# Performance work log

Measured on AMD Instinct MI355X. Metric: run time of the kernel, lower is better.

## Reference

```python
import jax, jax.numpy as jnp
import numpy as np

NUM_LAYERS = 6
D = 16           # physical_dim == bond_dim (required for multi-layer consistency)
B, S, FIN = 128, 2048, 128


def setup_inputs() -> dict:
    key = jax.random.key(0)
    k0, k1, k2, k3 = jax.random.split(key, 4)
    return {
        "sequence": jax.random.normal(k0, (B, S, FIN), jnp.float32),
        "W_emb": jax.random.normal(k1, (FIN, D), jnp.float32) * 0.05,
        "b_emb": jnp.zeros((D,), jnp.float32),
        "u": jax.random.normal(k2, (NUM_LAYERS, D, D, D, D), jnp.float32) * 0.1,
        "w": jax.random.normal(k3, (NUM_LAYERS, D, D, D), jnp.float32) * 0.1,
    }


def _ent_entropy(sA, sB):
    # sA: (B, pA, d), sB: (B, pB, d)
    corr = jnp.einsum('bik,bjk->bij', sA, sB)          # (B, pA, pB)
    s = jnp.linalg.svd(corr, compute_uv=False)          # (B, min(pA,pB))
    sn = s / (jnp.sum(s, axis=1, keepdims=True) + 1e-8)
    return -jnp.sum(sn * jnp.log(sn + 1e-8), axis=1)    # (B,)


def _phi_q(sites):
    # sites: (B, n, d), n >= 4 and even
    n = sites.shape[1]
    mid = n // 2
    S_int = _ent_entropy(sites[:, :mid], sites[:, mid:])
    A, Bp = sites[:, :mid], sites[:, mid:]
    S1 = _ent_entropy(A[:, :mid // 2], A[:, mid // 2:])
    S2 = _ent_entropy(Bp[:, :(n - mid) // 2], Bp[:, (n - mid) // 2:])
    return jnp.maximum(S_int - (S1 + S2), 0.0)


def _apply_layer(sites, u_l, w_l):
    # sites: (B, n, d) with n even. Disentangle adjacent pairs, then coarse-grain.
    b, n, d = sites.shape
    s = sites.reshape(b, n // 2, 2, d)
    # disentangler: einsum('ijkl,bi,bj->bkl') batched over pairs p
    comb = jnp.einsum('ijkl,bpi,bpj->bpkl', u_l, s[:, :, 0], s[:, :, 1])
    o1 = comb.mean(axis=3)   # mean over l -> (b, p, k)
    o2 = comb.mean(axis=2)   # mean over k -> (b, p, l)
    # isometry acts on consecutive disentangled pairs (o1_i, o2_i)
    return jnp.einsum('aij,bpi,bpj->bpa', w_l, o1, o2)  # (b, n//2, bond)


def reference(sequence, W_emb, b_emb, u, w):
    emb = sequence @ W_emb + b_emb                       # (B, S, D)
    norm = jnp.linalg.norm(emb, axis=-1, keepdims=True)
    sites = emb / jnp.maximum(norm, 1e-12)               # F.normalize(dim=-1)
    for l in range(NUM_LAYERS):
        sites = _apply_layer(sites, u[l], w[l])
    phi_q = _phi_q(sites)
    return sites, phi_q
```

## Files before the change

### kernel.cpp

```cpp
#include <hip/hip_runtime.h>
#include <hip/hip_bf16.h>
#include <math.h>

#define BATCH 128
#define SEQ   2048
#define FIN   128
#define DD    16
#define NLAYERS 6
#define SST   20

#define BUFA_F  (BATCH*SEQ*DD)
#define BUFB_F  (BATCH*(SEQ/2)*DD)
#define COEF_OFF (BUFA_F + BUFB_F)
#define ENT_OFF  (COEF_OFF + NLAYERS*12288)

__global__ __launch_bounds__(256) void k_prep(const float* __restrict__ u,
                                              const float* __restrict__ w,
                                              float* __restrict__ coef) {
    int l  = blockIdx.x;
    int ij = threadIdx.x;
    const float* ub = u + (size_t)l*65536 + (size_t)ij*256;
    float a1[16], a2[16];
#pragma unroll
    for (int k = 0; k < 16; ++k) { a1[k] = 0.0f; a2[k] = 0.0f; }
#pragma unroll
    for (int k = 0; k < 16; ++k) {
#pragma unroll
        for (int z = 0; z < 16; ++z) {
            float v = ub[k*16 + z];
            a1[k] += v;
            a2[z] += v;
        }
    }
    float* ucb = coef + (size_t)l*12288 + ij*32;
#pragma unroll
    for (int k = 0; k < 16; ++k) {
        ucb[k]      = a1[k]*(1.0f/16.0f);
        ucb[16 + k] = a2[k]*(1.0f/16.0f);
    }
    const float* wb = w + (size_t)l*4096;
    float* wtb = coef + (size_t)l*12288 + 8192 + ij*16;
#pragma unroll
    for (int a = 0; a < 16; ++a) wtb[a] = wb[a*256 + ij];
}

__global__ __launch_bounds__(256) void k_embed(const float* __restrict__ seq,
                                               const float* __restrict__ W,
                                               const float* __restrict__ bias,
                                               float* __restrict__ out) {
    __shared__ float wl[2048];
    int t = threadIdx.x;
    for (int x = t; x < 2048; x += 256) wl[x] = W[x];
    int q = t & 3;
    size_t row = ((size_t)blockIdx.x*256 + t) >> 2;
    float acc[4];
    {
        float4 bv = *(const float4*)(bias + q*4);
        acc[0] = bv.x; acc[1] = bv.y; acc[2] = bv.z; acc[3] = bv.w;
    }
    __syncthreads();

    const float4* rp = (const float4*)seq + row*32;
#pragma unroll 8
    for (int kk = 0; kk < 32; ++kk) {
        float4 rv = rp[kk];
        float rc[4] = { rv.x, rv.y, rv.z, rv.w };
#pragma unroll
        for (int c = 0; c < 4; ++c) {
            float4 wv = *(const float4*)&wl[(kk*4 + c)*16 + q*4];
            float s = rc[c];
            acc[0] = fmaf(s, wv.x, acc[0]);
            acc[1] = fmaf(s, wv.y, acc[1]);
            acc[2] = fmaf(s, wv.z, acc[2]);
            acc[3] = fmaf(s, wv.w, acc[3]);
        }
    }
    float p = 0.0f;
#pragma unroll
    for (int j = 0; j < 4; ++j) p = fmaf(acc[j], acc[j], p);
    p += __shfl_xor(p, 1);
    p += __shfl_xor(p, 2);
    float inv = 1.0f / fmaxf(sqrtf(p), 1e-12f);
    *(float4*)(out + row*16 + q*4) = make_float4(acc[0]*inv, acc[1]*inv,
                                                 acc[2]*inv, acc[3]*inv);
}

__global__ __launch_bounds__(256) void k_layer(const float* __restrict__ in,
                                               float* __restrict__ outp,
                                               const float* __restrict__ coefl) {
    __shared__ float cbuf[8192];
    __shared__ float spl[64*36];
    int t = threadIdx.x;
    int og = t & 7, pg = t >> 3;
    int lane = t & 63, base = lane & ~7;

    const float4* wtf = (const float4*)(coefl + 8192);
    float4 wr0 = wtf[0*256 + t];
    float4 wr1 = wtf[1*256 + t];
    float4 wr2 = wtf[2*256 + t];
    float4 wr3 = wtf[3*256 + t];

    {
        const float4* ucf = (const float4*)coefl;
        float4* c4 = (float4*)cbuf;
#pragma unroll
        for (int it = 0; it < 8; ++it) c4[it*256 + t] = ucf[it*256 + t];
    }
    {
        const float4* ing = (const float4*)in + (size_t)blockIdx.x*512;
        float4 v0 = ing[t];
        float4 v1 = ing[t + 256];
        *(float4*)&spl[(t >> 3)*36 + (t & 7)*4]        = v0;
        *(float4*)&spl[((t >> 3) + 32)*36 + (t & 7)*4] = v1;
    }
    __syncthreads();

    float s1v[2][16];
#pragma unroll
    for (int pp = 0; pp < 2; ++pp) {
        int p = pg + pp*32;
#pragma unroll
        for (int g = 0; g < 4; ++g) {
            float4 v = *(const float4*)&spl[p*36 + 16 + g*4];
            s1v[pp][g*4+0]=v.x; s1v[pp][g*4+1]=v.y; s1v[pp][g*4+2]=v.z; s1v[pp][g*4+3]=v.w;
        }
    }

    float accv[2][4];
    accv[0][0]=0.f; accv[0][1]=0.f; accv[0][2]=0.f; accv[0][3]=0.f;
    accv[1][0]=0.f; accv[1][1]=0.f; accv[1][2]=0.f; accv[1][3]=0.f;

    for (int i = 0; i < 16; ++i) {
        float s0a = spl[pg*36 + i];
        float s0b = spl[(pg + 32)*36 + i];
        const float4* uc = (const float4*)&cbuf[i*512] + og;
#pragma unroll
        for (int j = 0; j < 16; ++j) {
            float4 cv = uc[j*8];
            float pa = s0a * s1v[0][j];
            float pb = s0b * s1v[1][j];
            accv[0][0] = fmaf(pa, cv.x, accv[0][0]);
            accv[0][1] = fmaf(pa, cv.y, accv[0][1]);
            accv[0][2] = fmaf(pa, cv.z, accv[0][2]);
            accv[0][3] = fmaf(pa, cv.w, accv[0][3]);
            accv[1][0] = fmaf(pb, cv.x, accv[1][0]);
            accv[1][1] = fmaf(pb, cv.y, accv[1][1]);
            accv[1][2] = fmaf(pb, cv.z, accv[1][2]);
            accv[1][3] = fmaf(pb, cv.w, accv[1][3]);
        }
    }
    __syncthreads();
    {
        float4* c4 = (float4*)cbuf;
        c4[0*256 + t] = wr0;
        c4[1*256 + t] = wr1;
        c4[2*256 + t] = wr2;
        c4[3*256 + t] = wr3;
    }
    __syncthreads();

    float o2f[2][16];
#pragma unroll
    for (int j = 0; j < 16; ++j) {
        int src = base + 4 + (j >> 2);
        o2f[0][j] = __shfl(accv[0][j & 3], src, 64);
        o2f[1][j] = __shfl(accv[1][j & 3], src, 64);
    }

    float r0a = 0.f, r1a = 0.f, r0b = 0.f, r1b = 0.f;
    for (int grp = 0; grp < 4; ++grp) {
#pragma unroll
        for (int c = 0; c < 4; ++c) {
            float o1a = __shfl(accv[0][c], base + grp, 64);
            float o1b = __shfl(accv[1][c], base + grp, 64);
            const float2* wrow = (const float2*)&cbuf[(grp*4 + c)*256] + og;
#pragma unroll
            for (int j = 0; j < 16; ++j) {
                float2 wv = wrow[j*8];
                float qa = o1a * o2f[0][j];
                float qb = o1b * o2f[1][j];
                r0a = fmaf(qa, wv.x, r0a);
                r1a = fmaf(qa, wv.y, r1a);
                r0b = fmaf(qb, wv.x, r0b);
                r1b = fmaf(qb, wv.y, r1b);
            }
        }
    }

    size_t gp = (size_t)blockIdx.x*64;
    *(float2*)&outp[(gp + pg)*16 + og*2]      = make_float2(r0a, r1a);
    *(float2*)&outp[(gp + pg + 32)*16 + og*2] = make_float2(r0b, r1b);
}

template<int P, bool LAST>
__device__ __forceinline__ void layer_body(float* sL, const float* coef,
                                           float* outp, int npg, int t, int bid) {
    int og = t & 7, pg = t >> 3;
    int lane = t & 63, base = lane & ~7;
    bool act = pg < npg;

    float accv[P][4];
    float s1v[P][16];
#pragma unroll
    for (int pp = 0; pp < P; ++pp) { accv[pp][0]=0.f; accv[pp][1]=0.f; accv[pp][2]=0.f; accv[pp][3]=0.f; }

    if (act) {
#pragma unroll
        for (int pp = 0; pp < P; ++pp) {
            int r = 2*(pg + pp*32) + 1;
#pragma unroll
            for (int g = 0; g < 4; ++g) {
                float4 v = *(const float4*)&sL[r*SST + g*4];
                s1v[pp][g*4+0]=v.x; s1v[pp][g*4+1]=v.y; s1v[pp][g*4+2]=v.z; s1v[pp][g*4+3]=v.w;
            }
        }
        for (int i = 0; i < 16; ++i) {
            float s0[P];
#pragma unroll
            for (int pp = 0; pp < P; ++pp) s0[pp] = sL[(2*(pg + pp*32))*SST + i];
            const float4* uc = (const float4*)&coef[i*512] + og;
#pragma unroll
            for (int j = 0; j < 16; ++j) {
                float4 cv = uc[j*8];
#pragma unroll
                for (int pp = 0; pp < P; ++pp) {
                    float p = s0[pp] * s1v[pp][j];
                    accv[pp][0] = fmaf(p, cv.x, accv[pp][0]);
                    accv[pp][1] = fmaf(p, cv.y, accv[pp][1]);
                    accv[pp][2] = fmaf(p, cv.z, accv[pp][2]);
                    accv[pp][3] = fmaf(p, cv.w, accv[pp][3]);
                }
            }
        }
    }
    __syncthreads();

    if (act) {
        float o2f[P][16];
#pragma unroll
        for (int j = 0; j < 16; ++j) {
            int src = base + 4 + (j >> 2);
#pragma unroll
            for (int pp = 0; pp < P; ++pp)
                o2f[pp][j] = __shfl(accv[pp][j & 3], src, 64);
        }
        float r0[P], r1[P];
#pragma unroll
        for (int pp = 0; pp < P; ++pp) { r0[pp] = 0.f; r1[pp] = 0.f; }
        for (int grp = 0; grp < 4; ++grp) {
#pragma unroll
            for (int c = 0; c < 4; ++c) {
                float o1i[P];
#pragma unroll
                for (int pp = 0; pp < P; ++pp)
                    o1i[pp] = __shfl(accv[pp][c], base + grp, 64);
#pragma unroll
                for (int j = 0; j < 16; ++j) {
                    float2 wv = *(const float2*)&coef[8192 + ((grp*4+c)*16 + j)*16 + og*2];
#pragma unroll
                    for (int pp = 0; pp < P; ++pp) {
                        float q = o1i[pp] * o2f[pp][j];
                        r0[pp] = fmaf(q, wv.x, r0[pp]);
                        r1[pp] = fmaf(q, wv.y, r1[pp]);
                    }
                }
            }
        }
        if (LAST) {
#pragma unroll
            for (int pp = 0; pp < P; ++pp) {
                int p = pg + pp*32;
                *(float2*)&outp[((size_t)bid*32 + p)*16 + og*2] = make_float2(r0[pp], r1[pp]);
            }
        } else {
#pragma unroll
            for (int pp = 0; pp < P; ++pp) {
                int p = pg + pp*32;
                *(float2*)&sL[p*SST + og*2] = make_float2(r0[pp], r1[pp]);
            }
        }
    }
    __syncthreads();
}

__global__ __launch_bounds__(256) void k_tail(const float* __restrict__ in,
                                              const float* __restrict__ coefg,
                                              float* __restrict__ outp) {
    __shared__ float coef[12288];
    __shared__ float sL[256*SST];
    int t = threadIdx.x, bid = blockIdx.x;

    const float4* in4 = (const float4*)in + (size_t)bid*1024;
#pragma unroll
    for (int it = 0; it < 4; ++it) {
        int f = it*256 + t;
        *(float4*)&sL[(f >> 2)*SST + (f & 3)*4] = in4[f];
    }
#pragma unroll 1
    for (int l = 0; l < 3; ++l) {
        const float4* src = (const float4*)(coefg + (size_t)(3 + l)*12288);
        __syncthreads();
        for (int x = t; x < 3072; x += 256) ((float4*)coef)[x] = src[x];
        __syncthreads();
        switch (l) {
            case 0: layer_body<4,false>(sL, coef, outp, 32, t, bid); break;
            case 1: layer_body<2,false>(sL, coef, outp, 32, t, bid); break;
            case 2: layer_body<1,true >(sL, coef, outp, 32, t, bid); break;
        }
    }
}

__device__ __forceinline__ void rot_cs(float al, float be, float ga, float& c, float& s) {
    float ze = (be - al) / (2.0f * ga);
    float tt = copysignf(1.0f, ze) / (fabsf(ze) + sqrtf(1.0f + ze*ze));
    c = 1.0f / sqrtf(1.0f + tt*tt);
    s = c * tt;
}

__global__ __launch_bounds__(64) void k_phi(const float* __restrict__ sites,
                                            float* __restrict__ ent) {
    __shared__ float S[512];
    __shared__ float C[256];
    __shared__ float sv[16];
    int bid = blockIdx.x;
    int role = bid >> 7;
    int b = bid & 127;
    int t = threadIdx.x;
    const float* sp = sites + (size_t)b*512;

    if (role == 0) {
        for (int x = t; x < 512; x += 64) S[x] = sp[x];
        __syncthreads();
        for (int e = t; e < 256; e += 64) {
            int i = e & 15, j = e >> 4;
            float a = 0.0f;
            for (int k = 0; k < 16; ++k) a = fmaf(S[i*16+k], S[(16+j)*16+k], a);
            C[j*16 + i] = a;
        }
        __syncthreads();
        for (int sw = 0; sw < 12; ++sw) {
            for (int r = 0; r < 15; ++r) {
                int pr = t >> 3, sub = t & 7;
                int p, q;
                if (pr == 0) { p = 15; q = r; }
                else { p = (r + pr) % 15; q = (r + 15 - pr) % 15; }
                float u0 = C[p*16 + 2*sub],   u1v = C[p*16 + 2*sub + 1];
                float v0 = C[q*16 + 2*sub],   v1v = C[q*16 + 2*sub + 1];
                float al = u0*u0 + u1v*u1v;
                float be = v0*v0 + v1v*v1v;
                float ga = u0*v0 + u1v*v1v;
                al += __shfl_xor(al,1); al += __shfl_xor(al,2); al += __shfl_xor(al,4);
                be += __shfl_xor(be,1); be += __shfl_xor(be,2); be += __shfl_xor(be,4);
                ga += __shfl_xor(ga,1); ga += __shfl_xor(ga,2); ga += __shfl_xor(ga,4);
                if (ga != 0.0f) {
                    float c, s; rot_cs(al, be, ga, c, s);
                    C[p*16 + 2*sub]     = fmaf(c, u0, -s*v0);
                    C[p*16 + 2*sub + 1] = fmaf(c, u1v, -s*v1v);
                    C[q*16 + 2*sub]     = fmaf(s, u0,  c*v0);
                    C[q*16 + 2*sub + 1] = fmaf(s, u1v, c*v1v);
                }
                __syncthreads();
            }
        }
        if (t < 16) {
            float s2 = 0.0f;
            for (int rr = 0; rr < 16; ++rr) { float v = C[t*16+rr]; s2 = fmaf(v, v, s2); }
            sv[t] = sqrtf(s2);
        }
        __syncthreads();
        if (t == 0) {
            float sum = 0.0f;
            for (int i2 = 0; i2 < 16; ++i2) sum += sv[i2];
            float den = sum + 1e-8f;
            float e2 = 0.0f;
            for (int i2 = 0; i2 < 16; ++i2) {
                float sn = sv[i2] / den;
                e2 -= sn * logf(sn + 1e-8f);
            }
            ent[b] = e2;
        }
    } else {
        int ro = (role == 1) ? 0 : 256;
        for (int x = t; x < 256; x += 64) S[x] = sp[ro + x];
        __syncthreads();
        if (t < 64) {
            int i = t & 7, j = t >> 3;
            float a = 0.0f;
            for (int k = 0; k < 16; ++k) a = fmaf(S[i*16+k], S[(8+j)*16+k], a);
            C[j*8 + i] = a;
        }
        __syncthreads();
        for (int sw = 0; sw < 12; ++sw) {
            for (int r = 0; r < 7; ++r) {
                if (t < 32) {
                    int pr = t >> 3, sub = t & 7;
                    int p, q;
                    if (pr == 0) { p = 7; q = r; }
                    else { p = (r + pr) % 7; q = (r + 7 - pr) % 7; }
                    float uu = C[p*8 + sub], vv = C[q*8 + sub];
                    float al = uu*uu, be = vv*vv, ga = uu*vv;
                    al += __shfl_xor(al,1); al += __shfl_xor(al,2); al += __shfl_xor(al,4);
                    be += __shfl_xor(be,1); be += __shfl_xor(be,2); be += __shfl_xor(be,4);
                    ga += __shfl_xor(ga,1); ga += __shfl_xor(ga,2); ga += __shfl_xor(ga,4);
                    if (ga != 0.0f) {
                        float c, s; rot_cs(al, be, ga, c, s);
                        C[p*8 + sub] = fmaf(c, uu, -s*vv);
                        C[q*8 + sub] = fmaf(s, uu,  c*vv);
                    }
                }
                __syncthreads();
            }
        }
        if (t < 8) {
            float s2 = 0.0f;
            for (int rr = 0; rr < 8; ++rr) { float v = C[t*8+rr]; s2 = fmaf(v, v, s2); }
            sv[t] = sqrtf(s2);
        }
        __syncthreads();
        if (t == 0) {
            float sum = 0.0f;
            for (int i2 = 0; i2 < 8; ++i2) sum += sv[i2];
            float den = sum + 1e-8f;
            float e2 = 0.0f;
            for (int i2 = 0; i2 < 8; ++i2) {
                float sn = sv[i2] / den;
                e2 -= sn * logf(sn + 1e-8f);
            }
            ent[role*128 + b] = e2;
        }
    }
}

__global__ __launch_bounds__(128) void k_phi2(const float* __restrict__ ent,
                                              float* __restrict__ phi) {
    int b = threadIdx.x;
    phi[b] = fmaxf(ent[b] - (ent[128 + b] + ent[256 + b]), 0.0f);
}

extern "C" void kernel_launch(void* const* d_in, const int* in_sizes, int n_in,
                              void* d_out, int out_size, void* d_ws, size_t ws_size,
                              hipStream_t stream) {
    const float* seq  = (const float*)d_in[0];
    const float* W    = (const float*)d_in[1];
    const float* bias = (const float*)d_in[2];
    const float* u    = (const float*)d_in[3];
    const float* w    = (const float*)d_in[4];
    float* out = (float*)d_out;
    float* ws  = (float*)d_ws;

    float* bufA  = ws;
    float* bufB  = ws + BUFA_F;
    float* coefw = ws + COEF_OFF;
    float* entb  = ws + ENT_OFF;

    k_prep <<<NLAYERS, 256, 0, stream>>>(u, w, coefw);
    k_embed<<<(BATCH*SEQ*4)/256, 256, 0, stream>>>(seq, W, bias, bufA);

    k_layer<<<2048, 256, 0, stream>>>(bufA, bufB, coefw + 0*12288);
    k_layer<<<1024, 256, 0, stream>>>(bufB, bufA, coefw + 1*12288);
    k_layer<<< 512, 256, 0, stream>>>(bufA, bufB, coefw + 2*12288);
    k_tail <<< 128, 256, 0, stream>>>(bufB, coefw, out);

    k_phi <<<3*BATCH, 64, 0, stream>>>(out, entb);
    k_phi2<<<1, 128, 0, stream>>>(entb, out + BATCH*32*DD);
}
```

Baseline: 232.3 us.

## Merge prep into embed kernel, stage rows in LDS, cut Jacobi sweeps

Folds the coefficient-prep kernel into the embedding kernel as six extra blocks, removing one launch. The embedding now loads 64 input rows per block into padded shared memory with coalesced float4 reads, instead of each thread striding through global memory. The one-sided Jacobi SVD sweep count in the phi kernel also drops from 12 to 8, which risks less converged singular values. The larger shared-memory footprint per block may lower occupancy in the bandwidth-bound embed stage.

```diff
diff --git a/kernel.cpp b/kernel.cpp
--- a/kernel.cpp
+++ b/kernel.cpp
@@ -8,51 +8,63 @@
 #define DD    16
 #define NLAYERS 6
 #define SST   20
+#define SWEEPS 8
 
 #define BUFA_F  (BATCH*SEQ*DD)
 #define BUFB_F  (BATCH*(SEQ/2)*DD)
 #define COEF_OFF (BUFA_F + BUFB_F)
 #define ENT_OFF  (COEF_OFF + NLAYERS*12288)
 
-__global__ __launch_bounds__(256) void k_prep(const float* __restrict__ u,
-                                              const float* __restrict__ w,
-                                              float* __restrict__ coef) {
-    int l  = blockIdx.x;
-    int ij = threadIdx.x;
-    const float* ub = u + (size_t)l*65536 + (size_t)ij*256;
-    float a1[16], a2[16];
-#pragma unroll
-    for (int k = 0; k < 16; ++k) { a1[k] = 0.0f; a2[k] = 0.0f; }
-#pragma unroll
-    for (int k = 0; k < 16; ++k) {
-#pragma unroll
-        for (int z = 0; z < 16; ++z) {
-            float v = ub[k*16 + z];
-            a1[k] += v;
-            a2[z] += v;
-        }
-    }
-    float* ucb = coef + (size_t)l*12288 + ij*32;
-#pragma unroll
-    for (int k = 0; k < 16; ++k) {
-        ucb[k]      = a1[k]*(1.0f/16.0f);
-        ucb[16 + k] = a2[k]*(1.0f/16.0f);
-    }
-    const float* wb = w + (size_t)l*4096;
-    float* wtb = coef + (size_t)l*12288 + 8192 + ij*16;
-#pragma unroll
-    for (int a = 0; a < 16; ++a) wtb[a] = wb[a*256 + ij];
-}
-
-__global__ __launch_bounds__(256) void k_embed(const float* __restrict__ seq,
+__global__ __launch_bounds__(256) void k_front(const float* __restrict__ seq,
                                                const float* __restrict__ W,
                                                const float* __restrict__ bias,
+                                               const float* __restrict__ u,
+                                               const float* __restrict__ w,
+                                               float* __restrict__ coef,
                                                float* __restrict__ out) {
-    __shared__ float wl[2048];
+    __shared__ float sW[2048];
+    __shared__ float sR[64*132];
     int t = threadIdx.x;
-    for (int x = t; x < 2048; x += 256) wl[x] = W[x];
-    int q = t & 3;
-    size_t row = ((size_t)blockIdx.x*256 + t) >> 2;
+    if (blockIdx.x < 6) {
+        int l  = blockIdx.x;
+        int ij = t;
+        const float* ub = u + (size_t)l*65536 + (size_t)ij*256;
+        float a1[16], a2[16];
+#pragma unroll
+        for (int k = 0; k < 16; ++k) { a1[k] = 0.0f; a2[k] = 0.0f; }
+#pragma unroll
+        for (int k = 0; k < 16; ++k) {
+#pragma unroll
+            for (int z = 0; z < 16; ++z) {
+                float v = ub[k*16 + z];
+                a1[k] += v;
+                a2[z] += v;
+            }
+        }
+        float* ucb = coef + (size_t)l*12288 + ij*32;
+#pragma unroll
+        for (int k = 0; k < 16; ++k) {
+            ucb[k]      = a1[k]*(1.0f/16.0f);
+            ucb[16 + k] = a2[k]*(1.0f/16.0f);
+        }
+        const float* wb = w + (size_t)l*4096;
+        float* wtb = coef + (size_t)l*12288 + 8192 + ij*16;
+#pragma unroll
+        for (int a = 0; a < 16; ++a) wtb[a] = wb[a*256 + ij];
+        return;
+    }
+    size_t rowbase = (size_t)(blockIdx.x - 6) * 64;
+    for (int x = t; x < 2048; x += 256) sW[x] = W[x];
+    {
+        const float4* seq4 = (const float4*)seq + rowbase*32;
+#pragma unroll
+        for (int it = 0; it < 8; ++it) {
+            int idx = t + it*256;
+            int r = idx >> 5, kk = idx & 31;
+            *(float4*)&sR[r*132 + kk*4] = seq4[idx];
+        }
+    }
+    int q = t & 3, lr = t >> 2;
     float acc[4];
     {
         float4 bv = *(const float4*)(bias + q*4);
@@ -60,14 +72,13 @@
     }
     __syncthreads();
 
-    const float4* rp = (const float4*)seq + row*32;
 #pragma unroll 8
     for (int kk = 0; kk < 32; ++kk) {
-        float4 rv = rp[kk];
+        float4 rv = *(const float4*)&sR[lr*132 + kk*4];
         float rc[4] = { rv.x, rv.y, rv.z, rv.w };
 #pragma unroll
         for (int c = 0; c < 4; ++c) {
-            float4 wv = *(const float4*)&wl[(kk*4 + c)*16 + q*4];
+            float4 wv = *(const float4*)&sW[(kk*4 + c)*16 + q*4];
             float s = rc[c];
             acc[0] = fmaf(s, wv.x, acc[0]);
             acc[1] = fmaf(s, wv.y, acc[1]);
@@ -81,8 +92,8 @@
     p += __shfl_xor(p, 1);
     p += __shfl_xor(p, 2);
     float inv = 1.0f / fmaxf(sqrtf(p), 1e-12f);
-    *(float4*)(out + row*16 + q*4) = make_float4(acc[0]*inv, acc[1]*inv,
-                                                 acc[2]*inv, acc[3]*inv);
+    *(float4*)(out + (rowbase + lr)*16 + q*4) = make_float4(acc[0]*inv, acc[1]*inv,
+                                                            acc[2]*inv, acc[3]*inv);
 }
 
 __global__ __launch_bounds__(256) void k_layer(const float* __restrict__ in,
@@ -338,7 +349,7 @@
             C[j*16 + i] = a;
         }
         __syncthreads();
-        for (int sw = 0; sw < 12; ++sw) {
+        for (int sw = 0; sw < SWEEPS; ++sw) {
             for (int r = 0; r < 15; ++r) {
                 int pr = t >> 3, sub = t & 7;
                 int p, q;
@@ -390,7 +401,7 @@
             C[j*8 + i] = a;
         }
         __syncthreads();
-        for (int sw = 0; sw < 12; ++sw) {
+        for (int sw = 0; sw < SWEEPS; ++sw) {
             for (int r = 0; r < 7; ++r) {
                 if (t < 32) {
                     int pr = t >> 3, sub = t & 7;
@@ -453,8 +464,7 @@
     float* coefw = ws + COEF_OFF;
     float* entb  = ws + ENT_OFF;
 
-    k_prep <<<NLAYERS, 256, 0, stream>>>(u, w, coefw);
-    k_embed<<<(BATCH*SEQ*4)/256, 256, 0, stream>>>(seq, W, bias, bufA);
+    k_front<<<6 + (BATCH*SEQ)/64, 256, 0, stream>>>(seq, W, bias, u, w, coefw, bufA);
 
     k_layer<<<2048, 256, 0, stream>>>(bufA, bufB, coefw + 0*12288);
     k_layer<<<1024, 256, 0, stream>>>(bufB, bufA, coefw + 1*12288);
```

New measurement: 211.5 us. -9.0%, faster.
